# Optimization experiments

Hardware: AMD Instinct MI355X
Metric: run time of the kernel (lower is better)

Reference implementation:

```python
import jax, jax.numpy as jnp
import numpy as np

NUM_HEADS = 16


def setup_inputs() -> dict:
    key = jax.random.key(0)
    ks = jax.random.split(key, 5)
    B, S, D = 2, 2048, 2048
    scale = 1.0 / np.sqrt(D)
    return {
        "x": jax.random.normal(ks[0], (B, S, D), dtype=jnp.float32),
        "W_q": jax.random.normal(ks[1], (D, D), dtype=jnp.float32) * scale,
        "W_k": jax.random.normal(ks[2], (D, D), dtype=jnp.float32) * scale,
        "W_v": jax.random.normal(ks[3], (D, D), dtype=jnp.float32) * scale,
        "W_o": jax.random.normal(ks[4], (D, D), dtype=jnp.float32) * scale,
        "b_o": jnp.zeros((D,), dtype=jnp.float32),
    }


def reference(x, W_q, W_k, W_v, W_o, b_o):
    B, S, D = x.shape
    H = NUM_HEADS
    hd = D // H
    # projections, split into heads: [B, H, S, hd]
    q = (x @ W_q).reshape(B, S, H, hd).transpose(0, 2, 1, 3)
    k = (x @ W_k).reshape(B, S, H, hd).transpose(0, 2, 1, 3)
    v = (x @ W_v).reshape(B, S, H, hd).transpose(0, 2, 1, 3)
    # causal attention with explicit score matrix [B, H, S, S]
    scores = jnp.einsum("bhqd,bhkd->bhqk", q, k) / jnp.sqrt(jnp.asarray(hd, x.dtype))
    causal = jnp.tril(jnp.ones((S, S), dtype=bool))  # True = keep
    scores = jnp.where(causal, scores, -jnp.inf)
    weights = jax.nn.softmax(scores, axis=-1)
    ctx = jnp.einsum("bhqk,bhkd->bhqd", weights, v)
    ctx = ctx.transpose(0, 2, 1, 3).reshape(B, S, D)
    return ctx @ W_o + b_o
```

## Files before the change

### kernel.cpp

```cpp
#include <hip/hip_runtime.h>
#include <stdint.h>

#define SQ_S 2048
#define DIM 2048
#define NH 16
#define HD 128
#define NB 2
#define NROWS (NB * SQ_S)
#define NQKV (3 * DIM)
#define NQK (2 * DIM)

typedef __bf16 bf16x8 __attribute__((ext_vector_type(8)));
typedef float f32x4 __attribute__((ext_vector_type(4)));
typedef unsigned short u16;

__device__ __forceinline__ u16 f2bf(float f) {
    unsigned int u = __float_as_uint(f);
    u += 0x7FFF + ((u >> 16) & 1);
    return (u16)(u >> 16);
}

__device__ __forceinline__ void load_lds16(const u16* g, u16* lds) {
    __builtin_amdgcn_global_load_lds(
        (const __attribute__((address_space(1))) unsigned int*)(uintptr_t)g,
        (__attribute__((address_space(3))) unsigned int*)(unsigned int)(uintptr_t)lds,
        16, 0, 0);
}

__global__ __launch_bounds__(256) void cast_x_kernel(const float* __restrict__ in,
                                                     u16* __restrict__ out) {
    int i = (blockIdx.x * 256 + threadIdx.x) * 4;
    float4 v = *(const float4*)(in + i);
    ushort4 o;
    o.x = f2bf(v.x); o.y = f2bf(v.y); o.z = f2bf(v.z); o.w = f2bf(v.w);
    *(ushort4*)(out + i) = o;
}

__global__ __launch_bounds__(256) void transpose_w_kernel(
    const float* __restrict__ w0, const float* __restrict__ w1,
    const float* __restrict__ w2, const float* __restrict__ w3,
    u16* __restrict__ o0, u16* __restrict__ o1,
    u16* __restrict__ o2, u16* __restrict__ o3) {
    __shared__ u16 tile[64][65];
    int z = blockIdx.z;
    const float* in = z == 0 ? w0 : z == 1 ? w1 : z == 2 ? w2 : w3;
    u16* out = z == 0 ? o0 : z == 1 ? o1 : z == 2 ? o2 : o3;
    int r0 = blockIdx.y * 64, c0 = blockIdx.x * 64;
    int t = threadIdx.x;
#pragma unroll
    for (int i = 0; i < 16; ++i) {
        int idx = i * 256 + t;
        int r = idx >> 6, c = idx & 63;
        tile[r][c] = f2bf(in[(size_t)(r0 + r) * DIM + c0 + c]);
    }
    __syncthreads();
#pragma unroll
    for (int i = 0; i < 4; ++i) {
        int idx = i * 256 + t;
        int oc = idx >> 4;
        int r4 = (idx & 15) * 4;
        ushort4 v;
        v.x = tile[r4 + 0][oc]; v.y = tile[r4 + 1][oc];
        v.z = tile[r4 + 2][oc]; v.w = tile[r4 + 3][oc];
        *(ushort4*)(out + (size_t)(c0 + oc) * DIM + r0 + r4) = v;
    }
}

#define NTK (DIM / 64)

__device__ __forceinline__ bf16x8 frag(const u16* half, int row, int lq) {
    return *(const bf16x8*)(half + row * 32 + (((lq + (row >> 1)) & 3) * 8));
}

__device__ __forceinline__ void stage_half(const u16* __restrict__ G, int grow0, int gcol0,
                                           u16* dst, int t) {
#pragma unroll
    for (int i = 0; i < 2; ++i) {
        int e = (i * 512 + t) * 8;
        int r = e >> 5;
        int c = ((t & 3) - (r >> 1)) & 3;
        load_lds16(G + (size_t)(grow0 + r) * DIM + gcol0 + c * 8, dst + e);
    }
}

#define HSZ (256 * 32)

__global__ __launch_bounds__(512) void gemm_qkv(const u16* __restrict__ A,
                                                const u16* __restrict__ Bt,
                                                u16* __restrict__ QKo,
                                                u16* __restrict__ Vt) {
    __shared__ u16 As[2][2][HSZ];
    __shared__ u16 Bs[2][2][HSZ];
    int bid = blockIdx.x;
    int wg = (bid & 7) * 48 + (bid >> 3);
    int bm = wg / 24, bn = wg % 24;
    int gm0 = bm * 256, gn0 = bn * 256;
    int t = threadIdx.x;
    int w = t >> 6, l = t & 63;
    int wm = w >> 2, wn = w & 3;
    int lr = l & 15, lq = l >> 4;
    int ar = wm * 128 + lr;
    int br = wn * 64 + lr;
    f32x4 acc[8][4] = {};
    bf16x8 af[4], bfr[4];

    stage_half(A,  gm0, 0,  As[0][0], t);
    stage_half(Bt, gn0, 0,  Bs[0][0], t);
    stage_half(A,  gm0, 32, As[0][1], t);
    stage_half(Bt, gn0, 32, Bs[0][1], t);
    asm volatile("s_waitcnt vmcnt(4)" ::: "memory");
    __builtin_amdgcn_s_barrier();

#pragma unroll 2
    for (int kt = 0; kt < NTK; ++kt) {
        int buf = kt & 1, nbuf = buf ^ 1;
        int ks = (kt + 1 < NTK) ? kt + 1 : kt;
#pragma unroll
        for (int kk = 0; kk < 2; ++kk) {
            const u16* ah = As[buf][kk];
            const u16* bh = Bs[buf][kk];
#pragma unroll
            for (int nf = 0; nf < 4; ++nf) bfr[nf] = frag(bh, br + nf * 16, lq);
#pragma unroll
            for (int mf = 0; mf < 4; ++mf) af[mf] = frag(ah, ar + mf * 16, lq);
            stage_half(A, gm0, ks * 64 + kk * 32, As[nbuf][kk], t);
            __builtin_amdgcn_s_barrier();
            __builtin_amdgcn_s_setprio(1);
#pragma unroll
            for (int mf = 0; mf < 4; ++mf)
#pragma unroll
                for (int nf = 0; nf < 4; ++nf)
                    acc[mf][nf] = __builtin_amdgcn_mfma_f32_16x16x32_bf16(af[mf], bfr[nf], acc[mf][nf], 0, 0, 0);
            __builtin_amdgcn_s_setprio(0);
            __builtin_amdgcn_s_barrier();
#pragma unroll
            for (int mf = 0; mf < 4; ++mf) af[mf] = frag(ah, ar + 64 + mf * 16, lq);
            stage_half(Bt, gn0, ks * 64 + kk * 32, Bs[nbuf][kk], t);
            asm volatile("s_waitcnt vmcnt(4)" ::: "memory");
            __builtin_amdgcn_s_barrier();
            __builtin_amdgcn_s_setprio(1);
#pragma unroll
            for (int mf = 0; mf < 4; ++mf)
#pragma unroll
                for (int nf = 0; nf < 4; ++nf)
                    acc[mf + 4][nf] = __builtin_amdgcn_mfma_f32_16x16x32_bf16(af[mf], bfr[nf], acc[mf + 4][nf], 0, 0, 0);
            __builtin_amdgcn_s_setprio(0);
            __builtin_amdgcn_s_barrier();
        }
    }
    asm volatile("s_waitcnt vmcnt(0)" ::: "memory");

    int c0g = gn0 + wn * 64;
    int r0g = gm0 + wm * 128;
    if (bn < 16) {
#pragma unroll
        for (int mf = 0; mf < 8; ++mf)
#pragma unroll
            for (int nf = 0; nf < 4; ++nf) {
                int col = c0g + nf * 16 + lr;
                int rowb = r0g + mf * 16 + lq * 4;
#pragma unroll
                for (int r = 0; r < 4; ++r)
                    QKo[(size_t)(rowb + r) * NQK + col] = f2bf(acc[mf][nf][r]);
            }
    } else {
#pragma unroll
        for (int mf = 0; mf < 8; ++mf)
#pragma unroll
            for (int nf = 0; nf < 4; ++nf) {
                int colv = c0g + nf * 16 + lr - 4096;
                int h = colv >> 7, dd = colv & 127;
                int rowb = r0g + mf * 16 + lq * 4;
                int b = rowb >> 11, s = rowb & 2047;
                ushort4 v4;
                v4.x = f2bf(acc[mf][nf][0]);
                v4.y = f2bf(acc[mf][nf][1]);
                v4.z = f2bf(acc[mf][nf][2]);
                v4.w = f2bf(acc[mf][nf][3]);
                *(ushort4*)(Vt + (((size_t)(b * NH + h) * HD + dd) * SQ_S + s)) = v4;
            }
    }
}

#define ASZ (256 * 32)
#define BSZ (128 * 32)

__device__ __forceinline__ void stage_b128(const u16* __restrict__ Bt, int gn0, int kt, int kk,
                                           u16* dst, int t) {
    int e = t * 8;
    int r = e >> 5;
    int c = ((t & 3) - (r >> 1)) & 3;
    load_lds16(Bt + (size_t)(gn0 + r) * DIM + kt * 64 + kk * 32 + c * 8, dst + e);
}

__device__ __forceinline__ void gemm_core(const u16* __restrict__ A, const u16* __restrict__ Bt,
                                          int gm0, int gn0, u16* As, u16* Bs,
                                          f32x4 acc[4][4]) {
    int t = threadIdx.x;
    int w = t >> 6, l = t & 63;
    int wm = w >> 1, wn = w & 1;
    int lr = l & 15, lq = l >> 4;
    int ar = wm * 64 + lr;
    int br = wn * 64 + lr;

    stage_half(A, gm0, 0, As + 0 * ASZ, t);
    stage_b128(Bt, gn0, 0, 0, Bs + 0 * BSZ, t);
    stage_half(A, gm0, 32, As + 1 * ASZ, t);
    stage_b128(Bt, gn0, 0, 1, Bs + 1 * BSZ, t);
    stage_half(A, gm0, 64, As + 2 * ASZ, t);
    stage_b128(Bt, gn0, 1, 0, Bs + 2 * BSZ, t);
    asm volatile("s_waitcnt vmcnt(6)" ::: "memory");
    __builtin_amdgcn_s_barrier();

#pragma unroll 2
    for (int kt = 0; kt < NTK; ++kt) {
        int buf = kt & 1, nbuf = buf ^ 1;
        const u16* a0 = As + (buf * 2 + 0) * ASZ;
        const u16* a1 = As + (buf * 2 + 1) * ASZ;
        const u16* b0 = Bs + (buf * 2 + 0) * BSZ;
        const u16* b1 = Bs + (buf * 2 + 1) * BSZ;
        bf16x8 af[4], bfr[4];

#pragma unroll
        for (int mf = 0; mf < 4; ++mf) af[mf] = frag(a0, ar + mf * 16, lq);
#pragma unroll
        for (int nf = 0; nf < 4; ++nf) bfr[nf] = frag(b0, br + nf * 16, lq);
        {
            int ks = (kt + 1 < NTK) ? kt + 1 : kt;
            stage_half(A, gm0, ks * 64 + 32, As + (nbuf * 2 + 1) * ASZ, t);
            stage_b128(Bt, gn0, ks, 1, Bs + (nbuf * 2 + 1) * BSZ, t);
        }
        asm volatile("s_waitcnt vmcnt(6)" ::: "memory");
        __builtin_amdgcn_s_barrier();
        __builtin_amdgcn_s_setprio(1);
#pragma unroll
        for (int mf = 0; mf < 4; ++mf)
#pragma unroll
            for (int nf = 0; nf < 4; ++nf)
                acc[mf][nf] = __builtin_amdgcn_mfma_f32_16x16x32_bf16(af[mf], bfr[nf], acc[mf][nf], 0, 0, 0);
        __builtin_amdgcn_s_setprio(0);
        __builtin_amdgcn_s_barrier();

#pragma unroll
        for (int mf = 0; mf < 4; ++mf) af[mf] = frag(a1, ar + mf * 16, lq);
#pragma unroll
        for (int nf = 0; nf < 4; ++nf) bfr[nf] = frag(b1, br + nf * 16, lq);
        {
            int ks = (kt + 2 < NTK) ? kt + 2 : kt;
            stage_half(A, gm0, ks * 64, As + (buf * 2 + 0) * ASZ, t);
            stage_b128(Bt, gn0, ks, 0, Bs + (buf * 2 + 0) * BSZ, t);
        }
        asm volatile("s_waitcnt vmcnt(6)" ::: "memory");
        __builtin_amdgcn_s_barrier();
        __builtin_amdgcn_s_setprio(1);
#pragma unroll
        for (int mf = 0; mf < 4; ++mf)
#pragma unroll
            for (int nf = 0; nf < 4; ++nf)
                acc[mf][nf] = __builtin_amdgcn_mfma_f32_16x16x32_bf16(af[mf], bfr[nf], acc[mf][nf], 0, 0, 0);
        __builtin_amdgcn_s_setprio(0);
        __builtin_amdgcn_s_barrier();
    }
    asm volatile("s_waitcnt vmcnt(0)" ::: "memory");
}

__global__ __launch_bounds__(512) void gemm_out(const u16* __restrict__ A,
                                                const u16* __restrict__ Bt,
                                                float* __restrict__ C,
                                                const float* __restrict__ bias) {
    __shared__ u16 As[4 * ASZ];
    __shared__ u16 Bs[4 * BSZ];
    int bid = blockIdx.x;
    int wg = (bid & 7) * 32 + (bid >> 3);
    int bm = wg >> 4, bn = wg & 15;
    f32x4 acc[4][4] = {};
    gemm_core(A, Bt, bm * 256, bn * 128, As, Bs, acc);

    int t = threadIdx.x, w = t >> 6, l = t & 63;
    int wm = w >> 1, wn = w & 1, lr = l & 15, lq = l >> 4;
    int r0 = bm * 256 + wm * 64;
    int c0 = bn * 128 + wn * 64;
#pragma unroll
    for (int mf = 0; mf < 4; ++mf)
#pragma unroll
        for (int nf = 0; nf < 4; ++nf) {
            int col = c0 + nf * 16 + lr;
            float bb = bias[col];
            int rowb = r0 + mf * 16 + lq * 4;
#pragma unroll
            for (int r = 0; r < 4; ++r)
                C[(size_t)(rowb + r) * DIM + col] = acc[mf][nf][r] + bb;
        }
}

__global__ __launch_bounds__(256) void attn_kernel(const u16* __restrict__ Q,
                                                   const u16* __restrict__ K,
                                                   const u16* __restrict__ Vt,
                                                   u16* __restrict__ ctx, int ldqk) {
    __shared__ u16 Kl[2][64 * 128];
    __shared__ u16 Vl[2][128 * 64];
    __shared__ u16 Pl[4][16 * 64];
    int t = threadIdx.x;
    int w = t >> 6, l = t & 63;
    int lr = l & 15, q = l >> 4, lk = q * 8;
    int bid = blockIdx.x;
    int r_  = bid >> 3;
    int px  = r_ & 15;
    int h   = (bid & 7) + ((r_ >> 4) & 1) * 8;
    int b   = r_ >> 5;
    const float scale = 0.08838834764831845f;
    int stK_gcol = (((t & 15) ^ (t >> 4)) * 8);
    int stV_gcol = (((t & 7) ^ ((t >> 3) & 7)) * 8);
    const u16* Kbase = K + (size_t)b * SQ_S * ldqk + h * HD;
    const u16* Vbase = Vt + ((size_t)(b * NH + h)) * HD * SQ_S;

#pragma unroll 1
    for (int pass = 0; pass < 2; ++pass) {
        int qt = pass == 0 ? px : 31 - px;
        int q0 = qt * 64;
        int njt = qt + 1;

        bf16x8 qf[4];
        {
            const u16* qp = Q + ((size_t)(b * SQ_S + q0 + w * 16 + lr)) * ldqk + h * HD;
#pragma unroll
            for (int kd = 0; kd < 4; ++kd)
                qf[kd] = *(const bf16x8*)(qp + kd * 32 + lk);
        }

        f32x4 o[8] = {};
        float l_r[4] = {0.f, 0.f, 0.f, 0.f};

        {
            int e = t * 8;
#pragma unroll
            for (int c = 0; c < 4; ++c) {
                int eK = c * 2048 + e;
                load_lds16(Kbase + (size_t)(eK >> 7) * ldqk + stK_gcol, Kl[0] + eK);
            }
#pragma unroll
            for (int c = 0; c < 4; ++c) {
                int eV = c * 2048 + e;
                load_lds16(Vbase + (size_t)(eV >> 6) * SQ_S + stV_gcol, Vl[0] + eV);
            }
        }

#pragma unroll 1
        for (int jt = 0; jt < njt; ++jt) {
            __syncthreads();
            if (jt + 1 < njt) {
                int j1 = (jt + 1) * 64;
                u16* Kd = Kl[(jt + 1) & 1];
                u16* Vd = Vl[(jt + 1) & 1];
                int e = t * 8;
#pragma unroll
                for (int c = 0; c < 4; ++c) {
                    int eK = c * 2048 + e;
                    load_lds16(Kbase + (size_t)(j1 + (eK >> 7)) * ldqk + stK_gcol, Kd + eK);
                }
#pragma unroll
                for (int c = 0; c < 4; ++c) {
                    int eV = c * 2048 + e;
                    load_lds16(Vbase + (size_t)(eV >> 6) * SQ_S + j1 + stV_gcol, Vd + eV);
                }
            }
            const u16* Kc = Kl[jt & 1];
            const u16* Vc = Vl[jt & 1];

            f32x4 s[4] = {};
#pragma unroll
            for (int kd = 0; kd < 4; ++kd) {
#pragma unroll
                for (int nt = 0; nt < 4; ++nt) {
                    bf16x8 kb = *(const bf16x8*)(Kc + (nt * 16 + lr) * 128 +
                                                 (((kd * 4 + q) ^ lr) * 8));
                    s[nt] = __builtin_amdgcn_mfma_f32_16x16x32_bf16(qf[kd], kb, s[nt], 0, 0, 0);
                }
            }
            bool diag = (jt == qt);
            float rs[4] = {0.f, 0.f, 0.f, 0.f};
            float pv[4][4];
#pragma unroll
            for (int nt = 0; nt < 4; ++nt)
#pragma unroll
                for (int r = 0; r < 4; ++r) {
                    float v = s[nt][r] * scale - 6.0f;
                    if (diag && (nt * 16 + lr > w * 16 + q * 4 + r)) v = -1.0e30f;
                    float pp = __expf(v);
                    pv[nt][r] = pp;
                    rs[r] += pp;
                }
#pragma unroll
            for (int d = 1; d < 16; d <<= 1)
#pragma unroll
                for (int r = 0; r < 4; ++r)
                    rs[r] += __shfl_xor(rs[r], d, 64);
#pragma unroll
            for (int r = 0; r < 4; ++r)
                l_r[r] += rs[r];
            u16* pw = Pl[w];
#pragma unroll
            for (int nt = 0; nt < 4; ++nt)
#pragma unroll
                for (int r = 0; r < 4; ++r) {
                    int prow = q * 4 + r;
                    int pcol = nt * 16 + lr;
                    pw[prow * 64 + (((pcol >> 3) ^ (prow & 7)) * 8) + (pcol & 7)] = f2bf(pv[nt][r]);
                }
            asm volatile("s_waitcnt lgkmcnt(0)" ::: "memory");
#pragma unroll
            for (int kj = 0; kj < 2; ++kj) {
                bf16x8 pa = *(const bf16x8*)(pw + lr * 64 + (((kj * 4 + q) ^ (lr & 7)) * 8));
#pragma unroll
                for (int nd = 0; nd < 8; ++nd) {
                    bf16x8 vb = *(const bf16x8*)(Vc + (nd * 16 + lr) * 64 +
                                                 (((kj * 4 + q) ^ (lr & 7)) * 8));
                    o[nd] = __builtin_amdgcn_mfma_f32_16x16x32_bf16(pa, vb, o[nd], 0, 0, 0);
                }
            }
        }
        float li[4];
#pragma unroll
        for (int r = 0; r < 4; ++r) li[r] = 1.f / l_r[r];
#pragma unroll
        for (int nd = 0; nd < 8; ++nd)
#pragma unroll
            for (int r = 0; r < 4; ++r) {
                int row = q0 + w * 16 + q * 4 + r;
                int col = h * HD + nd * 16 + lr;
                ctx[((size_t)(b * SQ_S + row)) * DIM + col] = f2bf(o[nd][r] * li[r]);
            }
        __syncthreads();
    }
}

extern "C" void kernel_launch(void* const* d_in, const int* in_sizes, int n_in,
                              void* d_out, int out_size, void* d_ws, size_t ws_size,
                              hipStream_t stream) {
    const float* x  = (const float*)d_in[0];
    const float* Wq = (const float*)d_in[1];
    const float* Wk = (const float*)d_in[2];
    const float* Wv = (const float*)d_in[3];
    const float* Wo = (const float*)d_in[4];
    const float* bo = (const float*)d_in[5];
    float* out = (float*)d_out;

    char* p = (char*)d_ws;
    const size_t SZ_ACT = (size_t)NROWS * DIM * 2;
    const size_t SZ_W   = (size_t)DIM * DIM * 2;
    u16* Xb   = (u16*)(p);
    u16* Wqkv = (u16*)(p + SZ_ACT);
    u16* Wot  = (u16*)(p + SZ_ACT + 3 * SZ_W);
    u16* QK   = (u16*)(p + SZ_ACT + 4 * SZ_W);
    u16* Vt   = (u16*)(p + 3 * SZ_ACT + 4 * SZ_W);
    u16* Cx   = (u16*)(p + 4 * SZ_ACT + 4 * SZ_W);

    cast_x_kernel<<<(NROWS * DIM) / 1024, 256, 0, stream>>>(x, Xb);
    transpose_w_kernel<<<dim3(DIM / 64, DIM / 64, 4), 256, 0, stream>>>(
        Wq, Wk, Wv, Wo,
        Wqkv, Wqkv + (size_t)DIM * DIM, Wqkv + 2 * (size_t)DIM * DIM, Wot);
    gemm_qkv<<<384, 512, 0, stream>>>(Xb, Wqkv, QK, Vt);
    attn_kernel<<<512, 256, 0, stream>>>(QK, QK + DIM, Vt, Cx, NQK);
    gemm_out<<<256, 512, 0, stream>>>(Cx, Wot, out, bo);
}
```

Baseline: 366.0 us.

## Software-pipeline LDS fragment loads with MFMA in QKV and output GEMMs

Restructures the main loops of both GEMM kernels so LDS fragments for the next sub-step are read into a second register set while MFMAs run on the current one, and the first fragments are prefetched before the loop. The QKV kernel splits its accumulator into low and high halves with four A-fragment register sets. The output GEMM drops from three staged k-halves in flight to two and uses a tighter vmcnt. The aim is to hide LDS read latency and cut barrier stalls between MFMA bursts, at the cost of more VGPRs and a shallower global-load prefetch in gemm_out.

```diff
diff --git a/kernel.cpp b/kernel.cpp
--- a/kernel.cpp
+++ b/kernel.cpp
@@ -82,6 +82,16 @@
         load_lds16(G + (size_t)(grow0 + r) * DIM + gcol0 + c * 8, dst + e);
     }
 }
+
+#define MMA4x4(ACC, AF, BF)                                                              \
+    do {                                                                                 \
+        __builtin_amdgcn_s_setprio(1);                                                   \
+        _Pragma("unroll") for (int mf_ = 0; mf_ < 4; ++mf_)                              \
+            _Pragma("unroll") for (int nf_ = 0; nf_ < 4; ++nf_)                          \
+                ACC[mf_][nf_] = __builtin_amdgcn_mfma_f32_16x16x32_bf16(                 \
+                    AF[mf_], BF[nf_], ACC[mf_][nf_], 0, 0, 0);                           \
+        __builtin_amdgcn_s_setprio(0);                                                   \
+    } while (0)
 
 #define HSZ (256 * 32)
 
@@ -101,8 +111,9 @@
     int lr = l & 15, lq = l >> 4;
     int ar = wm * 128 + lr;
     int br = wn * 64 + lr;
-    f32x4 acc[8][4] = {};
-    bf16x8 af[4], bfr[4];
+    f32x4 accL[4][4] = {};
+    f32x4 accH[4][4] = {};
+    bf16x8 afA[4], afB[4], afC[4], afD[4], bf0[4], bf1[4];
 
     stage_half(A,  gm0, 0,  As[0][0], t);
     stage_half(Bt, gn0, 0,  Bs[0][0], t);
@@ -110,43 +121,43 @@
     stage_half(Bt, gn0, 32, Bs[0][1], t);
     asm volatile("s_waitcnt vmcnt(4)" ::: "memory");
     __builtin_amdgcn_s_barrier();
+#pragma unroll
+    for (int i = 0; i < 4; ++i) {
+        afA[i] = frag(As[0][0], ar + i * 16, lq);
+        bf0[i] = frag(Bs[0][0], br + i * 16, lq);
+    }
 
 #pragma unroll 2
     for (int kt = 0; kt < NTK; ++kt) {
         int buf = kt & 1, nbuf = buf ^ 1;
         int ks = (kt + 1 < NTK) ? kt + 1 : kt;
 #pragma unroll
-        for (int kk = 0; kk < 2; ++kk) {
-            const u16* ah = As[buf][kk];
-            const u16* bh = Bs[buf][kk];
-#pragma unroll
-            for (int nf = 0; nf < 4; ++nf) bfr[nf] = frag(bh, br + nf * 16, lq);
-#pragma unroll
-            for (int mf = 0; mf < 4; ++mf) af[mf] = frag(ah, ar + mf * 16, lq);
-            stage_half(A, gm0, ks * 64 + kk * 32, As[nbuf][kk], t);
-            __builtin_amdgcn_s_barrier();
-            __builtin_amdgcn_s_setprio(1);
-#pragma unroll
-            for (int mf = 0; mf < 4; ++mf)
-#pragma unroll
-                for (int nf = 0; nf < 4; ++nf)
-                    acc[mf][nf] = __builtin_amdgcn_mfma_f32_16x16x32_bf16(af[mf], bfr[nf], acc[mf][nf], 0, 0, 0);
-            __builtin_amdgcn_s_setprio(0);
-            __builtin_amdgcn_s_barrier();
-#pragma unroll
-            for (int mf = 0; mf < 4; ++mf) af[mf] = frag(ah, ar + 64 + mf * 16, lq);
-            stage_half(Bt, gn0, ks * 64 + kk * 32, Bs[nbuf][kk], t);
-            asm volatile("s_waitcnt vmcnt(4)" ::: "memory");
-            __builtin_amdgcn_s_barrier();
-            __builtin_amdgcn_s_setprio(1);
-#pragma unroll
-            for (int mf = 0; mf < 4; ++mf)
-#pragma unroll
-                for (int nf = 0; nf < 4; ++nf)
-                    acc[mf + 4][nf] = __builtin_amdgcn_mfma_f32_16x16x32_bf16(af[mf], bfr[nf], acc[mf + 4][nf], 0, 0, 0);
-            __builtin_amdgcn_s_setprio(0);
-            __builtin_amdgcn_s_barrier();
-        }
+        for (int i = 0; i < 4; ++i) afB[i] = frag(As[buf][0], ar + 64 + i * 16, lq);
+        stage_half(A,  gm0, ks * 64, As[nbuf][0], t);
+        stage_half(Bt, gn0, ks * 64, Bs[nbuf][0], t);
+        MMA4x4(accL, afA, bf0);
+        asm volatile("s_waitcnt vmcnt(4)" ::: "memory");
+        __builtin_amdgcn_s_barrier();
+#pragma unroll
+        for (int i = 0; i < 4; ++i) {
+            bf1[i] = frag(Bs[buf][1], br + i * 16, lq);
+            afC[i] = frag(As[buf][1], ar + i * 16, lq);
+        }
+        stage_half(A,  gm0, ks * 64 + 32, As[nbuf][1], t);
+        stage_half(Bt, gn0, ks * 64 + 32, Bs[nbuf][1], t);
+        MMA4x4(accH, afB, bf0);
+#pragma unroll
+        for (int i = 0; i < 4; ++i) afD[i] = frag(As[buf][1], ar + 64 + i * 16, lq);
+        MMA4x4(accL, afC, bf1);
+        asm volatile("s_waitcnt vmcnt(4)" ::: "memory");
+        __builtin_amdgcn_s_barrier();
+#pragma unroll
+        for (int i = 0; i < 4; ++i) {
+            bf0[i] = frag(Bs[nbuf][0], br + i * 16, lq);
+            afA[i] = frag(As[nbuf][0], ar + i * 16, lq);
+        }
+        MMA4x4(accH, afD, bf1);
+        __builtin_amdgcn_s_barrier();
     }
     asm volatile("s_waitcnt vmcnt(0)" ::: "memory");
 
@@ -154,31 +165,35 @@
     int r0g = gm0 + wm * 128;
     if (bn < 16) {
 #pragma unroll
-        for (int mf = 0; mf < 8; ++mf)
-#pragma unroll
-            for (int nf = 0; nf < 4; ++nf) {
-                int col = c0g + nf * 16 + lr;
-                int rowb = r0g + mf * 16 + lq * 4;
-#pragma unroll
-                for (int r = 0; r < 4; ++r)
-                    QKo[(size_t)(rowb + r) * NQK + col] = f2bf(acc[mf][nf][r]);
-            }
+        for (int half = 0; half < 2; ++half)
+#pragma unroll
+            for (int mf = 0; mf < 4; ++mf)
+#pragma unroll
+                for (int nf = 0; nf < 4; ++nf) {
+                    f32x4 v = half ? accH[mf][nf] : accL[mf][nf];
+                    int col = c0g + nf * 16 + lr;
+                    int rowb = r0g + half * 64 + mf * 16 + lq * 4;
+#pragma unroll
+                    for (int r = 0; r < 4; ++r)
+                        QKo[(size_t)(rowb + r) * NQK + col] = f2bf(v[r]);
+                }
     } else {
 #pragma unroll
-        for (int mf = 0; mf < 8; ++mf)
-#pragma unroll
-            for (int nf = 0; nf < 4; ++nf) {
-                int colv = c0g + nf * 16 + lr - 4096;
-                int h = colv >> 7, dd = colv & 127;
-                int rowb = r0g + mf * 16 + lq * 4;
-                int b = rowb >> 11, s = rowb & 2047;
-                ushort4 v4;
-                v4.x = f2bf(acc[mf][nf][0]);
-                v4.y = f2bf(acc[mf][nf][1]);
-                v4.z = f2bf(acc[mf][nf][2]);
-                v4.w = f2bf(acc[mf][nf][3]);
-                *(ushort4*)(Vt + (((size_t)(b * NH + h) * HD + dd) * SQ_S + s)) = v4;
-            }
+        for (int half = 0; half < 2; ++half)
+#pragma unroll
+            for (int mf = 0; mf < 4; ++mf)
+#pragma unroll
+                for (int nf = 0; nf < 4; ++nf) {
+                    f32x4 v = half ? accH[mf][nf] : accL[mf][nf];
+                    int colv = c0g + nf * 16 + lr - 4096;
+                    int h = colv >> 7, dd = colv & 127;
+                    int rowb = r0g + half * 64 + mf * 16 + lq * 4;
+                    int b = rowb >> 11, s = rowb & 2047;
+                    ushort4 v4;
+                    v4.x = f2bf(v[0]); v4.y = f2bf(v[1]);
+                    v4.z = f2bf(v[2]); v4.w = f2bf(v[3]);
+                    *(ushort4*)(Vt + (((size_t)(b * NH + h) * HD + dd) * SQ_S + s)) = v4;
+                }
     }
 }
 
@@ -202,63 +217,44 @@
     int lr = l & 15, lq = l >> 4;
     int ar = wm * 64 + lr;
     int br = wn * 64 + lr;
+    bf16x8 af0[4], af1[4], bq0[4], bq1[4];
 
     stage_half(A, gm0, 0, As + 0 * ASZ, t);
     stage_b128(Bt, gn0, 0, 0, Bs + 0 * BSZ, t);
     stage_half(A, gm0, 32, As + 1 * ASZ, t);
     stage_b128(Bt, gn0, 0, 1, Bs + 1 * BSZ, t);
-    stage_half(A, gm0, 64, As + 2 * ASZ, t);
-    stage_b128(Bt, gn0, 1, 0, Bs + 2 * BSZ, t);
-    asm volatile("s_waitcnt vmcnt(6)" ::: "memory");
+    asm volatile("s_waitcnt vmcnt(3)" ::: "memory");
     __builtin_amdgcn_s_barrier();
+#pragma unroll
+    for (int i = 0; i < 4; ++i) {
+        af0[i] = frag(As + 0 * ASZ, ar + i * 16, lq);
+        bq0[i] = frag(Bs + 0 * BSZ, br + i * 16, lq);
+    }
 
 #pragma unroll 2
     for (int kt = 0; kt < NTK; ++kt) {
         int buf = kt & 1, nbuf = buf ^ 1;
-        const u16* a0 = As + (buf * 2 + 0) * ASZ;
-        const u16* a1 = As + (buf * 2 + 1) * ASZ;
-        const u16* b0 = Bs + (buf * 2 + 0) * BSZ;
-        const u16* b1 = Bs + (buf * 2 + 1) * BSZ;
-        bf16x8 af[4], bfr[4];
-
-#pragma unroll
-        for (int mf = 0; mf < 4; ++mf) af[mf] = frag(a0, ar + mf * 16, lq);
-#pragma unroll
-        for (int nf = 0; nf < 4; ++nf) bfr[nf] = frag(b0, br + nf * 16, lq);
-        {
-            int ks = (kt + 1 < NTK) ? kt + 1 : kt;
-            stage_half(A, gm0, ks * 64 + 32, As + (nbuf * 2 + 1) * ASZ, t);
-            stage_b128(Bt, gn0, ks, 1, Bs + (nbuf * 2 + 1) * BSZ, t);
-        }
-        asm volatile("s_waitcnt vmcnt(6)" ::: "memory");
-        __builtin_amdgcn_s_barrier();
-        __builtin_amdgcn_s_setprio(1);
-#pragma unroll
-        for (int mf = 0; mf < 4; ++mf)
-#pragma unroll
-            for (int nf = 0; nf < 4; ++nf)
-                acc[mf][nf] = __builtin_amdgcn_mfma_f32_16x16x32_bf16(af[mf], bfr[nf], acc[mf][nf], 0, 0, 0);
-        __builtin_amdgcn_s_setprio(0);
-        __builtin_amdgcn_s_barrier();
-
-#pragma unroll
-        for (int mf = 0; mf < 4; ++mf) af[mf] = frag(a1, ar + mf * 16, lq);
-#pragma unroll
-        for (int nf = 0; nf < 4; ++nf) bfr[nf] = frag(b1, br + nf * 16, lq);
-        {
-            int ks = (kt + 2 < NTK) ? kt + 2 : kt;
-            stage_half(A, gm0, ks * 64, As + (buf * 2 + 0) * ASZ, t);
-            stage_b128(Bt, gn0, ks, 0, Bs + (buf * 2 + 0) * BSZ, t);
-        }
-        asm volatile("s_waitcnt vmcnt(6)" ::: "memory");
-        __builtin_amdgcn_s_barrier();
-        __builtin_amdgcn_s_setprio(1);
-#pragma unroll
-        for (int mf = 0; mf < 4; ++mf)
-#pragma unroll
-            for (int nf = 0; nf < 4; ++nf)
-                acc[mf][nf] = __builtin_amdgcn_mfma_f32_16x16x32_bf16(af[mf], bfr[nf], acc[mf][nf], 0, 0, 0);
-        __builtin_amdgcn_s_setprio(0);
+        int ks = (kt + 1 < NTK) ? kt + 1 : kt;
+        stage_half(A, gm0, ks * 64, As + (nbuf * 2 + 0) * ASZ, t);
+        stage_b128(Bt, gn0, ks, 0, Bs + (nbuf * 2 + 0) * BSZ, t);
+        asm volatile("s_waitcnt vmcnt(3)" ::: "memory");
+        __builtin_amdgcn_s_barrier();
+#pragma unroll
+        for (int i = 0; i < 4; ++i) {
+            af1[i] = frag(As + (buf * 2 + 1) * ASZ, ar + i * 16, lq);
+            bq1[i] = frag(Bs + (buf * 2 + 1) * BSZ, br + i * 16, lq);
+        }
+        MMA4x4(acc, af0, bq0);
+        stage_half(A, gm0, ks * 64 + 32, As + (nbuf * 2 + 1) * ASZ, t);
+        stage_b128(Bt, gn0, ks, 1, Bs + (nbuf * 2 + 1) * BSZ, t);
+        asm volatile("s_waitcnt vmcnt(3)" ::: "memory");
+        __builtin_amdgcn_s_barrier();
+#pragma unroll
+        for (int i = 0; i < 4; ++i) {
+            af0[i] = frag(As + (nbuf * 2 + 0) * ASZ, ar + i * 16, lq);
+            bq0[i] = frag(Bs + (nbuf * 2 + 0) * BSZ, br + i * 16, lq);
+        }
+        MMA4x4(acc, af1, bq1);
         __builtin_amdgcn_s_barrier();
     }
     asm volatile("s_waitcnt vmcnt(0)" ::: "memory");
```

Measured after the change: 364.6 us. About the same (-0.4%).
